# Performance work log

Measured on AMD Instinct MI355X. Metric: run time of the kernel, lower is better.

Reference implementation:

```python
import jax, jax.numpy as jnp
import numpy as np

SIDE = 9
STATE = SIDE * SIDE          # 81
NA = 5                       # stay, up, down, left, right
_MOVES = [(0, 0), (-1, 0), (1, 0), (0, -1), (0, 1)]

def _dest(s, a):
    r, c = divmod(s, SIDE)
    nr, nc = r + _MOVES[a][0], c + _MOVES[a][1]
    if 0 <= nr < SIDE and 0 <= nc < SIDE:
        return nr * SIDE + nc
    return s  # off-grid moves stay in place

# inflows[i] = all (s, a) with dest(s, a) == i; flattened as edge lists.
_src, _dst = [], []
for s in range(STATE):
    for a in range(NA):
        _src.append(s * NA + a)          # flat index into action_count[B, 81*5]
        _dst.append(_dest(s, a))
INFLOW_SRC = jnp.asarray(np.array(_src, dtype=np.int32))
INFLOW_DST = jnp.asarray(np.array(_dst, dtype=np.int32))


def setup_inputs() -> dict:
    key = jax.random.key(0)
    k1, k2, k3, k4, k5 = jax.random.split(key, 5)
    B = 131072
    obs = jax.random.uniform(k1, (B, 3 * STATE), dtype=jnp.float32)
    action_count = jax.random.uniform(k2, (B, STATE, NA), dtype=jnp.float32)
    W1 = jax.random.normal(k3, (STATE, 32), dtype=jnp.float32) * 0.1
    W2 = jax.random.normal(k4, (32, 32), dtype=jnp.float32) * 0.1
    W3 = jax.random.normal(k5, (32, 1), dtype=jnp.float32) * 0.1
    b3 = jnp.zeros((1,), dtype=jnp.float32)
    return {"obs": obs, "action_count": action_count,
            "W1": W1, "W2": W2, "W3": W3, "b3": b3}


def reference(obs, action_count, W1, W2, W3, b3):
    B = obs.shape[0]
    demand_count = obs[:, 2 * STATE:]                       # [B, 81]
    af = action_count.reshape(B, STATE * NA)                # [B, 405]
    # Vectorized replacement of the per-state gather+stack+reduce_sum loops:
    # next_state_count[b, i] = sum over (s,a) in inflows[i] of action_count[b, s, a]
    next_state_count = jnp.zeros((B, STATE), af.dtype).at[:, INFLOW_DST].add(af[:, INFLOW_SRC])
    # served_demand[b, i] = min(next_state_count[b, i], demand_count[b, i])
    served_demands = jnp.minimum(next_state_count, demand_count)
    immediate_reward = jnp.sum(served_demands, axis=1)      # [B]
    # value MLP on next_state_count (hidden dense layers have no bias)
    x = jax.nn.relu(next_state_count @ W1)
    x = jax.nn.relu(x @ W2)
    next_return = (x @ W3 + b3)[:, 0]                       # [B]
    symbolic_val = immediate_reward + next_return           # stack+reduce_sum
    return symbolic_val, immediate_reward, next_return, next_state_count
```

## Files before the change

### kernel.cpp

```cpp
#include <hip/hip_runtime.h>

#define SIDE 9
#define STATE 81
#define NA 5
#define NJ (STATE * NA)
#define H1 32
#define H2 32

#define CCH 27
#define BROWS 256
#define NAF 15
#define NCH 18
#define OBS_STRIDE (3 * STATE)

struct DstTab { int v[NJ]; };
constexpr DstTab make_dst() {
    DstTab t{};
    const int dr[NA] = {0, -1, 1, 0, 0};
    const int dc[NA] = {0, 0, 0, -1, 1};
    for (int s = 0; s < STATE; ++s) {
        int r = s / SIDE, c = s % SIDE;
        for (int a = 0; a < NA; ++a) {
            int nr = r + dr[a], nc = c + dc[a];
            int d = (nr >= 0 && nr < SIDE && nc >= 0 && nc < SIDE) ? nr * SIDE + nc : s;
            t.v[s * NA + a] = d;
        }
    }
    return t;
}
constexpr DstTab DST = make_dst();

__global__ __launch_bounds__(256) __attribute__((amdgpu_waves_per_eu(2, 2)))
void grid_vpn_kernel(
    const float* __restrict__ obs,
    const float* __restrict__ af,
    const float* __restrict__ W1,
    const float* __restrict__ W2,
    const float* __restrict__ W3,
    const float* __restrict__ b3,
    float* __restrict__ out,
    int B)
{
    __shared__ float lb[BROWS * CCH];

    const int tid = (int)threadIdx.x;
    const int r0  = (int)blockIdx.x * BROWS;
    const int Bm1 = B - 1;

    const int sr_r0 = tid / CCH;
    const int sr_c0 = tid - sr_r0 * CCH;

    float nsc[STATE];
#pragma unroll
    for (int d = 0; d < STATE; ++d) nsc[d] = 0.0f;
    float ir = 0.0f;

    float stg[CCH];

    auto loadRegs = [&](int c, float (&s)[CCH]) {
        const float* src = (c < NAF) ? af : obs;
        const int stride = (c < NAF) ? NJ : OBS_STRIDE;
        const int cb     = (c < NAF) ? c * CCH : 2 * STATE + (c - NAF) * CCH;
        int r = sr_r0, col = sr_c0;
#pragma unroll
        for (int t = 0; t < CCH; ++t) {
            int rr = r0 + r; rr = (rr <= Bm1) ? rr : Bm1;
            s[t] = src[(size_t)rr * stride + (cb + col)];
            col += 256 - 9 * CCH;
            int w = (col >= CCH) ? 1 : 0;
            r += 9 + w;
            col -= w ? CCH : 0;
        }
    };

    loadRegs(0, stg);
#pragma unroll
    for (int c = 0; c < NCH; ++c) {
#pragma unroll
        for (int t = 0; t < CCH; ++t) lb[t * BROWS + tid] = stg[t];
        if (c + 1 < NCH) loadRegs(c + 1, stg);
        asm volatile("s_waitcnt lgkmcnt(0)" ::: "memory");
        __builtin_amdgcn_s_barrier();
        if (c < NAF) {
#pragma unroll
            for (int j = 0; j < CCH; ++j)
                nsc[DST.v[c * CCH + j]] += lb[tid * CCH + j];
        } else {
#pragma unroll
            for (int j = 0; j < CCH; ++j)
                ir += fminf(nsc[(c - NAF) * CCH + j], lb[tid * CCH + j]);
        }
        asm volatile("s_waitcnt lgkmcnt(0)" ::: "memory");
        __builtin_amdgcn_s_barrier();
    }

    {
        const int wv = tid >> 6;
        const int ln = tid & 63;
        float* outns = out + 3 * (size_t)B + (size_t)r0 * STATE;
#pragma unroll
        for (int g = 0; g < 4; ++g) {
            if (wv == g) {
#pragma unroll
                for (int j = 0; j < STATE; ++j) lb[ln * STATE + j] = nsc[j];
            }
            asm volatile("s_waitcnt lgkmcnt(0)" ::: "memory");
            __builtin_amdgcn_s_barrier();
#pragma unroll
            for (int t = 0; t < 20; ++t)
                outns[g * 5184 + t * 256 + tid] = lb[t * 256 + tid];
            if (tid < 64) outns[g * 5184 + 5120 + tid] = lb[5120 + tid];
            asm volatile("s_waitcnt lgkmcnt(0)" ::: "memory");
            __builtin_amdgcn_s_barrier();
        }
    }

    float x1[H1];
#pragma unroll
    for (int j = 0; j < H1; ++j) x1[j] = 0.0f;
#pragma unroll
    for (int d = 0; d < STATE; ++d) {
        float v = nsc[d];
#pragma unroll
        for (int j = 0; j < H1; ++j) x1[j] = fmaf(v, W1[d * H1 + j], x1[j]);
    }
#pragma unroll
    for (int j = 0; j < H1; ++j) x1[j] = fmaxf(x1[j], 0.0f);

    float x2[H2];
#pragma unroll
    for (int j = 0; j < H2; ++j) x2[j] = 0.0f;
#pragma unroll
    for (int k = 0; k < H1; ++k) {
        float v = x1[k];
#pragma unroll
        for (int j = 0; j < H2; ++j) x2[j] = fmaf(v, W2[k * H2 + j], x2[j]);
    }
#pragma unroll
    for (int j = 0; j < H2; ++j) x2[j] = fmaxf(x2[j], 0.0f);

    float nr = b3[0];
#pragma unroll
    for (int k = 0; k < H2; ++k) nr = fmaf(x2[k], W3[k], nr);

    int b = r0 + tid;
    if (b < B) {
        out[b] = ir + nr;
        out[(size_t)B + b] = ir;
        out[2 * (size_t)B + b] = nr;
    }
}

extern "C" void kernel_launch(void* const* d_in, const int* in_sizes, int n_in,
                              void* d_out, int out_size, void* d_ws, size_t ws_size,
                              hipStream_t stream) {
    const float* obs = (const float*)d_in[0];
    const float* ac  = (const float*)d_in[1];
    const float* W1  = (const float*)d_in[2];
    const float* W2  = (const float*)d_in[3];
    const float* W3  = (const float*)d_in[4];
    const float* b3  = (const float*)d_in[5];
    float* out = (float*)d_out;

    int B = in_sizes[0] / (3 * STATE);
    int block = BROWS;
    int grid = (B + BROWS - 1) / BROWS;
    hipLaunchKernelGGL(grid_vpn_kernel, dim3(grid), dim3(block), 0, stream,
                       obs, ac, W1, W2, W3, b3, out, B);
}
```

Before: 398.6 us.

## Double-buffer LDS staging with two-deep register prefetch and fewer barriers

Splits the single LDS staging buffer into two ping-pong buffers and keeps two register staging arrays, so each chunk's global loads are issued two iterations ahead. Because consecutive chunks now use different buffers, the second barrier in each chunk loop and in the output-transpose loop can be dropped. Row offsets for the action_count loads are precomputed once as byte offsets to cut address arithmetic. The cost is doubled LDS use and higher register pressure, which could limit occupancy under the fixed waves-per-EU setting.

```diff
diff --git a/kernel.cpp b/kernel.cpp
--- a/kernel.cpp
+++ b/kernel.cpp
@@ -41,7 +41,7 @@
     float* __restrict__ out,
     int B)
 {
-    __shared__ float lb[BROWS * CCH];
+    __shared__ float buf[2][BROWS * CCH];
 
     const int tid = (int)threadIdx.x;
     const int r0  = (int)blockIdx.x * BROWS;
@@ -50,22 +50,33 @@
     const int sr_r0 = tid / CCH;
     const int sr_c0 = tid - sr_r0 * CCH;
 
-    float nsc[STATE];
-#pragma unroll
-    for (int d = 0; d < STATE; ++d) nsc[d] = 0.0f;
-    float ir = 0.0f;
-
-    float stg[CCH];
-
-    auto loadRegs = [&](int c, float (&s)[CCH]) {
-        const float* src = (c < NAF) ? af : obs;
-        const int stride = (c < NAF) ? NJ : OBS_STRIDE;
-        const int cb     = (c < NAF) ? c * CCH : 2 * STATE + (c - NAF) * CCH;
+    int offs[CCH];
+    {
         int r = sr_r0, col = sr_c0;
 #pragma unroll
         for (int t = 0; t < CCH; ++t) {
             int rr = r0 + r; rr = (rr <= Bm1) ? rr : Bm1;
-            s[t] = src[(size_t)rr * stride + (cb + col)];
+            offs[t] = (rr * NJ + col) * 4;
+            col += 256 - 9 * CCH;
+            int w = (col >= CCH) ? 1 : 0;
+            r += 9 + w;
+            col -= w ? CCH : 0;
+        }
+    }
+
+    const char* afc = reinterpret_cast<const char*>(af);
+    auto loadAF = [&](int c, float (&s)[CCH]) {
+#pragma unroll
+        for (int t = 0; t < CCH; ++t)
+            s[t] = *reinterpret_cast<const float*>(afc + offs[t] + c * CCH * 4);
+    };
+    auto loadDem = [&](int c, float (&s)[CCH]) {
+        const int cb = 2 * STATE + (c - NAF) * CCH;
+        int r = sr_r0, col = sr_c0;
+#pragma unroll
+        for (int t = 0; t < CCH; ++t) {
+            int rr = r0 + r; rr = (rr <= Bm1) ? rr : Bm1;
+            s[t] = obs[(size_t)rr * OBS_STRIDE + (cb + col)];
             col += 256 - 9 * CCH;
             int w = (col >= CCH) ? 1 : 0;
             r += 9 + w;
@@ -73,25 +84,38 @@
         }
     };
 
-    loadRegs(0, stg);
+    float nsc[STATE];
+#pragma unroll
+    for (int d = 0; d < STATE; ++d) nsc[d] = 0.0f;
+    float ir = 0.0f;
+
+    float stgA[CCH], stgB[CCH];
+
+    loadAF(0, stgA);
+    loadAF(1, stgB);
+
 #pragma unroll
     for (int c = 0; c < NCH; ++c) {
+        float (&stg)[CCH] = (c & 1) ? stgB : stgA;
+        float* lb = &buf[c & 1][0];
 #pragma unroll
         for (int t = 0; t < CCH; ++t) lb[t * BROWS + tid] = stg[t];
-        if (c + 1 < NCH) loadRegs(c + 1, stg);
+        if (c + 2 < NCH) {
+            if (c + 2 < NAF) loadAF(c + 2, stg);
+            else             loadDem(c + 2, stg);
+        }
         asm volatile("s_waitcnt lgkmcnt(0)" ::: "memory");
         __builtin_amdgcn_s_barrier();
+        const float* lr = &buf[c & 1][tid * CCH];
         if (c < NAF) {
 #pragma unroll
             for (int j = 0; j < CCH; ++j)
-                nsc[DST.v[c * CCH + j]] += lb[tid * CCH + j];
+                nsc[DST.v[c * CCH + j]] += lr[j];
         } else {
 #pragma unroll
             for (int j = 0; j < CCH; ++j)
-                ir += fminf(nsc[(c - NAF) * CCH + j], lb[tid * CCH + j]);
+                ir += fminf(nsc[(c - NAF) * CCH + j], lr[j]);
         }
-        asm volatile("s_waitcnt lgkmcnt(0)" ::: "memory");
-        __builtin_amdgcn_s_barrier();
     }
 
     {
@@ -100,6 +124,7 @@
         float* outns = out + 3 * (size_t)B + (size_t)r0 * STATE;
 #pragma unroll
         for (int g = 0; g < 4; ++g) {
+            float* lb = &buf[g & 1][0];
             if (wv == g) {
 #pragma unroll
                 for (int j = 0; j < STATE; ++j) lb[ln * STATE + j] = nsc[j];
@@ -110,8 +135,6 @@
             for (int t = 0; t < 20; ++t)
                 outns[g * 5184 + t * 256 + tid] = lb[t * 256 + tid];
             if (tid < 64) outns[g * 5184 + 5120 + tid] = lb[5120 + tid];
-            asm volatile("s_waitcnt lgkmcnt(0)" ::: "memory");
-            __builtin_amdgcn_s_barrier();
         }
     }
 
```

Measured after the change: 405.4 us. About the same (+1.7%).
